# Optimization experiments

Measured on AMD Instinct MI355X. Metric: run time of the kernel, lower is better.

Reference implementation:

```python
import jax, jax.numpy as jnp
import numpy as np

B, T, D, H = 2, 2048, 512, 8
HD = D // H
EPS = 1e-5


def setup_inputs() -> dict:
    key = jax.random.key(0)
    ks = jax.random.split(key, 8)
    s = 1.0 / np.sqrt(D)
    return {
        "x": jax.random.normal(ks[0], (B, T, D), dtype=jnp.float32),
        "Wq": jax.random.uniform(ks[1], (D, D), jnp.float32, -s, s),
        "bq": jnp.zeros((D,), jnp.float32),
        "Wk": jax.random.uniform(ks[2], (D, D), jnp.float32, -s, s),
        "bk": jnp.zeros((D,), jnp.float32),
        "Wv": jax.random.uniform(ks[3], (D, D), jnp.float32, -s, s),
        "bv": jnp.zeros((D,), jnp.float32),
        "gn_w": jnp.ones((D,), jnp.float32),
        "gn_b": jnp.zeros((D,), jnp.float32),
        "gamma": jnp.float32(0.9),
    }


def reference(x, Wq, bq, Wk, bk, Wv, bv, gn_w, gn_b, gamma):
    Bx, Tx, Dx = x.shape
    # projections (torch Linear: x @ W.T + b), split heads -> [B,H,T,hd]
    def proj(W, b):
        return (x @ W.T + b).reshape(Bx, Tx, H, HD).transpose(0, 2, 1, 3)
    Q, K, V = proj(Wq, bq), proj(Wk, bk), proj(Wv, bv)
    # retention scores with causal exponential decay mask
    attn = jnp.einsum("bhqd,bhkd->bhqk", Q, K)  # [B,H,T,T]
    idx = jnp.arange(Tx)
    diff = idx[:, None] - idx[None, :]
    # clamp negative exponents before pow to avoid inf (masked out anyway)
    decay = jnp.where(diff >= 0,
                      jnp.power(gamma, jnp.maximum(diff, 0).astype(jnp.float32)),
                      0.0)
    attn = attn * decay[None, None]
    out = jnp.einsum("bhqk,bhkd->bhqd", attn, V)  # [B,H,T,hd]
    out = out.transpose(0, 2, 1, 3)  # [B,T,H,hd]
    # GroupNorm over channels grouped by head; normalized over (T, hd) per (b, h)
    mean = out.mean(axis=(1, 3), keepdims=True)
    var = out.var(axis=(1, 3), keepdims=True)
    out = (out - mean) / jnp.sqrt(var + EPS)
    out = out.reshape(Bx, Tx, Dx) * gn_w + gn_b
    return out
```

## Files before the change

kernel.cpp:

```cpp
#include <hip/hip_runtime.h>
#include <math.h>

#define B_ 2
#define T_ 2048
#define D_ 512
#define H_ 8
#define HD_ 64
#define NG_ (B_*H_)
#define EPS_ 1e-5f

typedef __attribute__((ext_vector_type(8)))  short  short8;
typedef __attribute__((ext_vector_type(16))) float  floatx16;

__device__ inline floatx16 zero16() {
    floatx16 z;
#pragma unroll
    for (int i = 0; i < 16; i++) z[i] = 0.f;
    return z;
}

__device__ inline unsigned pack2bf(float a, float b) {
    unsigned ua = __float_as_uint(a), ub = __float_as_uint(b);
    ua = (ua + 0x7fffu + ((ua >> 16) & 1u)) >> 16;
    ub = (ub + 0x7fffu + ((ub >> 16) & 1u)) >> 16;
    return ua | (ub << 16);
}
__device__ inline short bf1(float a) {
    unsigned ua = __float_as_uint(a);
    return (short)((ua + 0x7fffu + ((ua >> 16) & 1u)) >> 16);
}

__global__ __launch_bounds__(256) void convert_kernel(
    const float* __restrict__ x,
    const float* __restrict__ Wq, const float* __restrict__ Wk, const float* __restrict__ Wv,
    short* __restrict__ xb, short* __restrict__ Wb)
{
    const int XN = 4096 * 512;
    const int WN = 512 * 512;
    size_t e = ((size_t)blockIdx.x * 256 + threadIdx.x) * 8;
    const float* src; short* dst;
    if (e < XN)               { src = x  + e;               dst = xb + e; }
    else if (e < XN + WN)     { src = Wq + (e - XN);        dst = Wb + (e - XN); }
    else if (e < XN + 2*WN)   { src = Wk + (e - XN - WN);   dst = Wb + (e - XN); }
    else                      { src = Wv + (e - XN - 2*WN); dst = Wb + (e - XN); }
    float4 a = *(const float4*)src;
    float4 b = *(const float4*)(src + 4);
    uint4 o;
    o.x = pack2bf(a.x, a.y); o.y = pack2bf(a.z, a.w);
    o.z = pack2bf(b.x, b.y); o.w = pack2bf(b.z, b.w);
    *(uint4*)dst = o;
}

__global__ __launch_bounds__(256) void proj_mfma(
    const short* __restrict__ xb, const short* __restrict__ Wb,
    const float* __restrict__ bq, const float* __restrict__ bk, const float* __restrict__ bv,
    short* __restrict__ Qo, short* __restrict__ Ko, short* __restrict__ Vto)
{
    __shared__ short Xs[2][64 * 64];
    __shared__ short Ws2[2][128 * 64];

    const int tid = threadIdx.x;
    const int w = tid >> 6, lane = tid & 63;
    const int hi = lane >> 5, ln = lane & 31;
    const int mt0 = blockIdx.x * 64;
    const int nt0 = blockIdx.y * 128;
    const int z = blockIdx.z;
    const bool isV = (z == 2);
    const float* bias = (z == 0) ? bq : (z == 1) ? bk : bv;
    const short* Wz = Wb + (size_t)z * 512 * 512;

    const int srow = tid >> 3;
    const int scol = (tid & 7) * 8;
    const int mh = w & 1, nh = w >> 1;

    floatx16 acc[2] = {zero16(), zero16()};

    auto stage = [&](int b, int k0) {
#pragma unroll
        for (int i = 0; i < 2; i++) {
            const short* gx = xb + (size_t)(mt0 + srow + i * 32) * 512 + k0 + scol;
            short* lx = &Xs[b][(srow + i * 32) * 64 + scol];
            __builtin_amdgcn_global_load_lds(
                (const __attribute__((address_space(1))) unsigned*)gx,
                (__attribute__((address_space(3))) unsigned*)lx, 16, 0, 0);
        }
#pragma unroll
        for (int i = 0; i < 4; i++) {
            const short* gw = Wz + (size_t)(nt0 + srow + i * 32) * 512 + k0 + scol;
            short* lw = &Ws2[b][(srow + i * 32) * 64 + scol];
            __builtin_amdgcn_global_load_lds(
                (const __attribute__((address_space(1))) unsigned*)gw,
                (__attribute__((address_space(3))) unsigned*)lw, 16, 0, 0);
        }
    };

    stage(0, 0);
    int buf = 0;
    for (int k0 = 0; k0 < 512; k0 += 64, buf ^= 1) {
        __syncthreads();
        if (k0 + 64 < 512) stage(buf ^ 1, k0 + 64);
#pragma unroll
        for (int kk = 0; kk < 4; kk++) {
            short8 xf = *(const short8*)(&Xs[buf][(mh * 32 + ln) * 64 + kk * 16 + hi * 8]);
            short8 wf[2];
#pragma unroll
            for (int s = 0; s < 2; s++)
                wf[s] = *(const short8*)(&Ws2[buf][(nh * 64 + s * 32 + ln) * 64 + kk * 16 + hi * 8]);
#pragma unroll
            for (int b = 0; b < 2; b++)
                acc[b] = isV
                    ? __builtin_amdgcn_mfma_f32_32x32x16_bf16(wf[b], xf, acc[b], 0, 0, 0)
                    : __builtin_amdgcn_mfma_f32_32x32x16_bf16(xf, wf[b], acc[b], 0, 0, 0);
        }
    }

    const int head = blockIdx.y * 2 + nh;

    if (!isV) {
        short* dst = (z == 0) ? Qo : Ko;
        float bias_v[2];
#pragma unroll
        for (int b = 0; b < 2; b++) bias_v[b] = bias[nt0 + nh * 64 + b * 32 + ln];
#pragma unroll
        for (int r = 0; r < 16; r++) {
            int m = mt0 + mh * 32 + (r & 3) + 8 * (r >> 2) + 4 * hi;
            int batch = m >> 11, t = m & (T_ - 1);
            size_t rowb = ((size_t)(batch * H_ + head) * T_ + t) * HD_;
#pragma unroll
            for (int b = 0; b < 2; b++)
                dst[rowb + b * 32 + ln] = bf1(acc[b][r] + bias_v[b]);
        }
    } else {
        const int m = mt0 + mh * 32 + ln;
        const int batch = m >> 11, t = m & (T_ - 1);
#pragma unroll
        for (int b = 0; b < 2; b++) {
#pragma unroll
            for (int r = 0; r < 16; r++) {
                int chan = nt0 + nh * 64 + b * 32 + (r & 3) + 8 * (r >> 2) + 4 * hi;
                int d = chan & (HD_ - 1);
                Vto[((size_t)(batch * H_ + head) * HD_ + d) * T_ + t] = bf1(acc[b][r] + bias[chan]);
            }
        }
    }
}

__global__ __launch_bounds__(256, 2) void retention_kernel(
    const short* __restrict__ Q, const short* __restrict__ K, const short* __restrict__ Vt,
    const float* __restrict__ gamma_p,
    float* __restrict__ out,
    float* __restrict__ stats)
{
    __shared__ float red[3][32 * 64];

    const int tid  = threadIdx.x;
    const int ks   = tid >> 6, lane = tid & 63;
    const int hi   = lane >> 5, ln = lane & 31;
    const int g    = blockIdx.x, qtt = blockIdx.y;
    const int q0   = qtt * 32;
    const int qt   = qtt >> 1;

    const float gamma = gamma_p[0];
    const float lg = logf(gamma);
    int kt0 = 0;
    if (lg < -1e-6f) {
        int maxd = (int)(-34.0f / lg) + 64;
        kt0 = qt - (maxd >> 6);
        if (kt0 < 0) kt0 = 0;
    }

    const short* Qbase = Q + ((size_t)g * T_ + q0 + ln) * HD_;
    short8 qf[4];
#pragma unroll
    for (int c = 0; c < 4; c++) qf[c] = *(const short8*)(Qbase + 16 * c + 8 * hi);

    const float Alane = __expf(lg * (float)(ln - 4 * hi));
    const float G32   = __expf(-lg * 32.0f);
    float Ea[4], Eb[4];
#pragma unroll
    for (int j = 0; j < 4; j++) { Ea[j] = __expf(-lg * (float)j); Eb[j] = __expf(-lg * (float)(8 * j)); }
    const int qrel = (qtt & 1) * 32 + ln;

    floatx16 oacc[2] = {zero16(), zero16()};

    int kt = kt0 + ((ks - kt0) & 3);
    short8 kf[2][4];
    if (kt <= qt) {
        const short* Kbase = K + ((size_t)g * T_ + kt * 64) * HD_;
#pragma unroll
        for (int kh = 0; kh < 2; kh++)
#pragma unroll
            for (int c = 0; c < 4; c++)
                kf[kh][c] = *(const short8*)(Kbase + (size_t)(kh * 32 + ln) * HD_ + 16 * c + 8 * hi);
    }

    for (; kt <= qt; kt += 4) {
        const int k0 = kt * 64;

        floatx16 st[2];
#pragma unroll
        for (int kh = 0; kh < 2; kh++) {
            floatx16 acc = zero16();
#pragma unroll
            for (int c = 0; c < 4; c++)
                acc = __builtin_amdgcn_mfma_f32_32x32x16_bf16(kf[kh][c], qf[c], acc, 0, 0, 0);
            st[kh] = acc;
        }

        short8 vf[4][2];
#pragma unroll
        for (int c = 0; c < 4; c++)
#pragma unroll
            for (int dh = 0; dh < 2; dh++)
                vf[c][dh] = *(const short8*)(Vt + ((size_t)g * HD_ + dh * 32 + ln) * T_ + k0 + 16 * c + 8 * hi);

        const int ktn = kt + 4;
        if (ktn <= qt) {
            const short* Kn = K + ((size_t)g * T_ + ktn * 64) * HD_;
#pragma unroll
            for (int kh = 0; kh < 2; kh++)
#pragma unroll
                for (int c = 0; c < 4; c++)
                    kf[kh][c] = *(const short8*)(Kn + (size_t)(kh * 32 + ln) * HD_ + 16 * c + 8 * hi);
        }

        const float Ckt = __expf(lg * (float)(q0 - k0));
        const float base0 = Alane * Ckt;
        const bool diag = (kt == qt);
#pragma unroll
        for (int kh = 0; kh < 2; kh++) {
            float bb = base0 * (kh ? G32 : 1.0f);
#pragma unroll
            for (int r = 0; r < 16; r++) {
                float v = st[kh][r] * (bb * Ea[r & 3] * Eb[r >> 2]);
                if (diag) {
                    int kloc = kh * 32 + (r & 3) + 8 * (r >> 2) + 4 * hi;
                    if (qrel < kloc) v = 0.f;
                }
                st[kh][r] = v;
            }
        }

#pragma unroll
        for (int c = 0; c < 4; c++) {
            const int kh = c >> 1, rb = 8 * (c & 1);
            unsigned p0 = pack2bf(st[kh][rb+0], st[kh][rb+1]);
            unsigned p1 = pack2bf(st[kh][rb+2], st[kh][rb+3]);
            unsigned p2 = pack2bf(st[kh][rb+4], st[kh][rb+5]);
            unsigned p3 = pack2bf(st[kh][rb+6], st[kh][rb+7]);
            unsigned t0s = (unsigned)__shfl_xor((int)(hi ? p0 : p2), 32, 64);
            unsigned t1s = (unsigned)__shfl_xor((int)(hi ? p1 : p3), 32, 64);
            uint4 aw;
            aw.x = hi ? t0s : p0;  aw.y = hi ? t1s : p1;
            aw.z = hi ? p2  : t0s; aw.w = hi ? p3  : t1s;
            short8 afr = *reinterpret_cast<short8*>(&aw);
#pragma unroll
            for (int dh = 0; dh < 2; dh++)
                oacc[dh] = __builtin_amdgcn_mfma_f32_32x32x16_bf16(afr, vf[c][dh], oacc[dh], 0, 0, 0);
        }
    }

    if (ks) {
        float* rp = &red[ks - 1][0];
#pragma unroll
        for (int dh = 0; dh < 2; dh++)
#pragma unroll
            for (int r = 0; r < 16; r++) {
                int qloc = (r & 3) + 8 * (r >> 2) + 4 * hi;
                rp[qloc * 64 + dh * 32 + ln] = oacc[dh][r];
            }
    }
    __syncthreads();
    if (ks == 0) {
        const int b = g >> 3, h = g & 7;
        float sm = 0.f, sq = 0.f;
#pragma unroll
        for (int dh = 0; dh < 2; dh++)
#pragma unroll
            for (int r = 0; r < 16; r++) {
                int qloc = (r & 3) + 8 * (r >> 2) + 4 * hi;
                int col = qloc * 64 + dh * 32 + ln;
                float v = oacc[dh][r] + red[0][col] + red[1][col] + red[2][col];
                int q = q0 + qloc;
                out[((size_t)(b * T_ + q)) * D_ + h * 64 + dh * 32 + ln] = v;
                sm += v; sq += v * v;
            }
        for (int off = 32; off > 0; off >>= 1) {
            sm += __shfl_down(sm, off);
            sq += __shfl_down(sq, off);
        }
        if (lane == 0) {
            atomicAdd(&stats[g], sm);
            atomicAdd(&stats[NG_ + g], sq);
        }
    }
}

__global__ __launch_bounds__(256) void norm_kernel(
    float* __restrict__ out, const float* __restrict__ stats,
    const float* __restrict__ gn_w, const float* __restrict__ gn_b)
{
    int idx4 = blockIdx.x * 256 + threadIdx.x;
    if (idx4 >= (B_ * T_ * D_) / 4) return;
    int base = idx4 * 4;
    int c0 = base & (D_ - 1);
    int b = base >> 20;
    int g = b * H_ + (c0 >> 6);
    const float invN = 1.f / (float)(T_ * HD_);
    float mean = stats[g] * invN;
    float var  = stats[NG_ + g] * invN - mean * mean;
    float inv  = rsqrtf(var + EPS_);
    float4 v = *(float4*)&out[base];
    float4 wv = *(const float4*)&gn_w[c0];
    float4 bv = *(const float4*)&gn_b[c0];
    v.x = (v.x - mean) * inv * wv.x + bv.x;
    v.y = (v.y - mean) * inv * wv.y + bv.y;
    v.z = (v.z - mean) * inv * wv.z + bv.z;
    v.w = (v.w - mean) * inv * wv.w + bv.w;
    *(float4*)&out[base] = v;
}

extern "C" void kernel_launch(void* const* d_in, const int* in_sizes, int n_in,
                              void* d_out, int out_size, void* d_ws, size_t ws_size,
                              hipStream_t stream)
{
    const float* x    = (const float*)d_in[0];
    const float* Wq   = (const float*)d_in[1];
    const float* bq   = (const float*)d_in[2];
    const float* Wk   = (const float*)d_in[3];
    const float* bk   = (const float*)d_in[4];
    const float* Wv   = (const float*)d_in[5];
    const float* bv   = (const float*)d_in[6];
    const float* gn_w = (const float*)d_in[7];
    const float* gn_b = (const float*)d_in[8];
    const float* gam  = (const float*)d_in[9];
    float* out = (float*)d_out;

    const size_t per = (size_t)B_ * H_ * T_ * HD_;
    float* stats = (float*)d_ws;
    short* Qw  = (short*)((char*)d_ws + 256);
    short* Kw  = Qw + per;
    short* Vtw = Kw + per;
    short* xb  = Vtw + per;
    short* Wb  = xb + per;

    hipMemsetAsync(stats, 0, 256, stream);
    convert_kernel<<<1408, 256, 0, stream>>>(x, Wq, Wk, Wv, xb, Wb);
    proj_mfma<<<dim3(64, 4, 3), 256, 0, stream>>>(xb, Wb, bq, bk, bv, Qw, Kw, Vtw);
    retention_kernel<<<dim3(16, 64), 256, 0, stream>>>(Qw, Kw, Vtw, gam, out, stats);
    norm_kernel<<<2048, 256, 0, stream>>>(out, stats, gn_w, gn_b);
}
```

Measured before the change: 128.0 us.

## Fuse all stages into one cooperative persistent kernel with grid syncs

Replaces the memset and four separate launches with a single cooperative kernel. Persistent blocks loop over the convert, projection, retention and norm work items, with grid-wide syncs between stages. The aim is to remove launch gaps and tail effects between kernels. In exchange it limits the grid to a few hundred resident blocks, adds grid-barrier cost, and may lower occupancy because the shared memory and register footprint now cover the largest stage.

```diff
diff --git a/kernel.cpp b/kernel.cpp
--- a/kernel.cpp
+++ b/kernel.cpp
@@ -1,5 +1,8 @@
 #include <hip/hip_runtime.h>
+#include <hip/hip_cooperative_groups.h>
 #include <math.h>
+
+namespace cg = cooperative_groups;
 
 #define B_ 2
 #define T_ 2048
@@ -30,294 +33,301 @@
     return (short)((ua + 0x7fffu + ((ua >> 16) & 1u)) >> 16);
 }
 
-__global__ __launch_bounds__(256) void convert_kernel(
+__global__ __launch_bounds__(256, 2) void mega_kernel(
     const float* __restrict__ x,
-    const float* __restrict__ Wq, const float* __restrict__ Wk, const float* __restrict__ Wv,
-    short* __restrict__ xb, short* __restrict__ Wb)
+    const float* __restrict__ Wq, const float* __restrict__ bq,
+    const float* __restrict__ Wk, const float* __restrict__ bk,
+    const float* __restrict__ Wv, const float* __restrict__ bv,
+    const float* __restrict__ gn_w, const float* __restrict__ gn_b,
+    const float* __restrict__ gamma_p,
+    float* __restrict__ out, float* __restrict__ stats,
+    short* __restrict__ xb, short* __restrict__ Wb,
+    short* __restrict__ Qo, short* __restrict__ Ko, short* __restrict__ Vto,
+    int G)
 {
-    const int XN = 4096 * 512;
-    const int WN = 512 * 512;
-    size_t e = ((size_t)blockIdx.x * 256 + threadIdx.x) * 8;
-    const float* src; short* dst;
-    if (e < XN)               { src = x  + e;               dst = xb + e; }
-    else if (e < XN + WN)     { src = Wq + (e - XN);        dst = Wb + (e - XN); }
-    else if (e < XN + 2*WN)   { src = Wk + (e - XN - WN);   dst = Wb + (e - XN); }
-    else                      { src = Wv + (e - XN - 2*WN); dst = Wb + (e - XN); }
-    float4 a = *(const float4*)src;
-    float4 b = *(const float4*)(src + 4);
-    uint4 o;
-    o.x = pack2bf(a.x, a.y); o.y = pack2bf(a.z, a.w);
-    o.z = pack2bf(b.x, b.y); o.w = pack2bf(b.z, b.w);
-    *(uint4*)dst = o;
-}
-
-__global__ __launch_bounds__(256) void proj_mfma(
-    const short* __restrict__ xb, const short* __restrict__ Wb,
-    const float* __restrict__ bq, const float* __restrict__ bk, const float* __restrict__ bv,
-    short* __restrict__ Qo, short* __restrict__ Ko, short* __restrict__ Vto)
-{
-    __shared__ short Xs[2][64 * 64];
-    __shared__ short Ws2[2][128 * 64];
+    cg::grid_group grid = cg::this_grid();
+    __shared__ __align__(16) char smem[49152];
 
     const int tid = threadIdx.x;
+    const int bid = blockIdx.x;
+    const int gsz = G * 256;
     const int w = tid >> 6, lane = tid & 63;
     const int hi = lane >> 5, ln = lane & 31;
-    const int mt0 = blockIdx.x * 64;
-    const int nt0 = blockIdx.y * 128;
-    const int z = blockIdx.z;
-    const bool isV = (z == 2);
-    const float* bias = (z == 0) ? bq : (z == 1) ? bk : bv;
-    const short* Wz = Wb + (size_t)z * 512 * 512;
-
-    const int srow = tid >> 3;
-    const int scol = (tid & 7) * 8;
-    const int mh = w & 1, nh = w >> 1;
-
-    floatx16 acc[2] = {zero16(), zero16()};
-
-    auto stage = [&](int b, int k0) {
-#pragma unroll
-        for (int i = 0; i < 2; i++) {
-            const short* gx = xb + (size_t)(mt0 + srow + i * 32) * 512 + k0 + scol;
-            short* lx = &Xs[b][(srow + i * 32) * 64 + scol];
-            __builtin_amdgcn_global_load_lds(
-                (const __attribute__((address_space(1))) unsigned*)gx,
-                (__attribute__((address_space(3))) unsigned*)lx, 16, 0, 0);
-        }
-#pragma unroll
-        for (int i = 0; i < 4; i++) {
-            const short* gw = Wz + (size_t)(nt0 + srow + i * 32) * 512 + k0 + scol;
-            short* lw = &Ws2[b][(srow + i * 32) * 64 + scol];
-            __builtin_amdgcn_global_load_lds(
-                (const __attribute__((address_space(1))) unsigned*)gw,
-                (__attribute__((address_space(3))) unsigned*)lw, 16, 0, 0);
-        }
-    };
-
-    stage(0, 0);
-    int buf = 0;
-    for (int k0 = 0; k0 < 512; k0 += 64, buf ^= 1) {
-        __syncthreads();
-        if (k0 + 64 < 512) stage(buf ^ 1, k0 + 64);
-#pragma unroll
-        for (int kk = 0; kk < 4; kk++) {
-            short8 xf = *(const short8*)(&Xs[buf][(mh * 32 + ln) * 64 + kk * 16 + hi * 8]);
-            short8 wf[2];
-#pragma unroll
-            for (int s = 0; s < 2; s++)
-                wf[s] = *(const short8*)(&Ws2[buf][(nh * 64 + s * 32 + ln) * 64 + kk * 16 + hi * 8]);
-#pragma unroll
-            for (int b = 0; b < 2; b++)
-                acc[b] = isV
-                    ? __builtin_amdgcn_mfma_f32_32x32x16_bf16(wf[b], xf, acc[b], 0, 0, 0)
-                    : __builtin_amdgcn_mfma_f32_32x32x16_bf16(xf, wf[b], acc[b], 0, 0, 0);
+
+    if (bid == 0 && tid < 32) stats[tid] = 0.f;
+    {
+        const int XN = 4096 * 512, WN = 512 * 512;
+        const int TOT8 = (XN + 3 * WN) / 8;
+        for (int e8 = bid * 256 + tid; e8 < TOT8; e8 += gsz) {
+            size_t e = (size_t)e8 * 8;
+            const float* src; short* dst;
+            if (e < XN)                 { src = x  + e;                 dst = xb + e; }
+            else if (e < XN + WN)       { src = Wq + (e - XN);          dst = Wb + (e - XN); }
+            else if (e < XN + 2u*WN)    { src = Wk + (e - XN - WN);     dst = Wb + (e - XN); }
+            else                        { src = Wv + (e - XN - 2*WN);   dst = Wb + (e - XN); }
+            float4 a = *(const float4*)src;
+            float4 b = *(const float4*)(src + 4);
+            uint4 o;
+            o.x = pack2bf(a.x, a.y); o.y = pack2bf(a.z, a.w);
+            o.z = pack2bf(b.x, b.y); o.w = pack2bf(b.z, b.w);
+            *(uint4*)dst = o;
         }
     }
-
-    const int head = blockIdx.y * 2 + nh;
-
-    if (!isV) {
-        short* dst = (z == 0) ? Qo : Ko;
-        float bias_v[2];
-#pragma unroll
-        for (int b = 0; b < 2; b++) bias_v[b] = bias[nt0 + nh * 64 + b * 32 + ln];
-#pragma unroll
-        for (int r = 0; r < 16; r++) {
-            int m = mt0 + mh * 32 + (r & 3) + 8 * (r >> 2) + 4 * hi;
-            int batch = m >> 11, t = m & (T_ - 1);
-            size_t rowb = ((size_t)(batch * H_ + head) * T_ + t) * HD_;
-#pragma unroll
-            for (int b = 0; b < 2; b++)
-                dst[rowb + b * 32 + ln] = bf1(acc[b][r] + bias_v[b]);
-        }
-    } else {
-        const int m = mt0 + mh * 32 + ln;
-        const int batch = m >> 11, t = m & (T_ - 1);
-#pragma unroll
-        for (int b = 0; b < 2; b++) {
-#pragma unroll
-            for (int r = 0; r < 16; r++) {
-                int chan = nt0 + nh * 64 + b * 32 + (r & 3) + 8 * (r >> 2) + 4 * hi;
-                int d = chan & (HD_ - 1);
-                Vto[((size_t)(batch * H_ + head) * HD_ + d) * T_ + t] = bf1(acc[b][r] + bias[chan]);
+    grid.sync();
+
+    {
+        short* XsB = (short*)smem;
+        short* WsB = (short*)(smem + 16384);
+        const int srow = tid >> 3, scol = (tid & 7) * 8;
+        const int mh = w & 1, nh = w >> 1;
+
+        for (int job = bid; job < 768; job += G) {
+            const int bx = job & 63, by = (job >> 6) & 3, z = job >> 8;
+            const int mt0 = bx * 64, nt0 = by * 128;
+            const bool isV = (z == 2);
+            const float* bias = (z == 0) ? bq : (z == 1) ? bk : bv;
+            const short* Wz = Wb + (size_t)z * 512 * 512;
+
+            __syncthreads();
+
+            floatx16 acc[2] = {zero16(), zero16()};
+
+            auto stage = [&](int b, int k0) {
+#pragma unroll
+                for (int i = 0; i < 2; i++) {
+                    const short* gx = xb + (size_t)(mt0 + srow + i * 32) * 512 + k0 + scol;
+                    short* lx = XsB + b * 4096 + (srow + i * 32) * 64 + scol;
+                    __builtin_amdgcn_global_load_lds(
+                        (const __attribute__((address_space(1))) unsigned*)gx,
+                        (__attribute__((address_space(3))) unsigned*)lx, 16, 0, 0);
+                }
+#pragma unroll
+                for (int i = 0; i < 4; i++) {
+                    const short* gw = Wz + (size_t)(nt0 + srow + i * 32) * 512 + k0 + scol;
+                    short* lw = WsB + b * 8192 + (srow + i * 32) * 64 + scol;
+                    __builtin_amdgcn_global_load_lds(
+                        (const __attribute__((address_space(1))) unsigned*)gw,
+                        (__attribute__((address_space(3))) unsigned*)lw, 16, 0, 0);
+                }
+            };
+
+            stage(0, 0);
+            int buf = 0;
+            for (int k0 = 0; k0 < 512; k0 += 64, buf ^= 1) {
+                __syncthreads();
+                if (k0 + 64 < 512) stage(buf ^ 1, k0 + 64);
+#pragma unroll
+                for (int kk = 0; kk < 4; kk++) {
+                    short8 xf = *(const short8*)(XsB + buf * 4096 + (mh * 32 + ln) * 64 + kk * 16 + hi * 8);
+                    short8 wf[2];
+#pragma unroll
+                    for (int s = 0; s < 2; s++)
+                        wf[s] = *(const short8*)(WsB + buf * 8192 + (nh * 64 + s * 32 + ln) * 64 + kk * 16 + hi * 8);
+#pragma unroll
+                    for (int b = 0; b < 2; b++)
+                        acc[b] = isV
+                            ? __builtin_amdgcn_mfma_f32_32x32x16_bf16(wf[b], xf, acc[b], 0, 0, 0)
+                            : __builtin_amdgcn_mfma_f32_32x32x16_bf16(xf, wf[b], acc[b], 0, 0, 0);
+                }
+            }
+
+            const int head = by * 2 + nh;
+            if (!isV) {
+                short* dst = (z == 0) ? Qo : Ko;
+                float bias_v[2];
+#pragma unroll
+                for (int b = 0; b < 2; b++) bias_v[b] = bias[nt0 + nh * 64 + b * 32 + ln];
+#pragma unroll
+                for (int r = 0; r < 16; r++) {
+                    int m = mt0 + mh * 32 + (r & 3) + 8 * (r >> 2) + 4 * hi;
+                    int batch = m >> 11, t = m & (T_ - 1);
+                    size_t rowb = ((size_t)(batch * H_ + head) * T_ + t) * HD_;
+#pragma unroll
+                    for (int b = 0; b < 2; b++)
+                        dst[rowb + b * 32 + ln] = bf1(acc[b][r] + bias_v[b]);
+                }
+            } else {
+                const int m = mt0 + mh * 32 + ln;
+                const int batch = m >> 11, t = m & (T_ - 1);
+#pragma unroll
+                for (int b = 0; b < 2; b++) {
+#pragma unroll
+                    for (int r = 0; r < 16; r++) {
+                        int chan = nt0 + nh * 64 + b * 32 + (r & 3) + 8 * (r >> 2) + 4 * hi;
+                        int d = chan & (HD_ - 1);
+                        Vto[((size_t)(batch * H_ + head) * HD_ + d) * T_ + t] = bf1(acc[b][r] + bias[chan]);
+                    }
+                }
             }
         }
     }
-}
-
-__global__ __launch_bounds__(256, 2) void retention_kernel(
-    const short* __restrict__ Q, const short* __restrict__ K, const short* __restrict__ Vt,
-    const float* __restrict__ gamma_p,
-    float* __restrict__ out,
-    float* __restrict__ stats)
-{
-    __shared__ float red[3][32 * 64];
-
-    const int tid  = threadIdx.x;
-    const int ks   = tid >> 6, lane = tid & 63;
-    const int hi   = lane >> 5, ln = lane & 31;
-    const int g    = blockIdx.x, qtt = blockIdx.y;
-    const int q0   = qtt * 32;
-    const int qt   = qtt >> 1;
-
-    const float gamma = gamma_p[0];
-    const float lg = logf(gamma);
-    int kt0 = 0;
-    if (lg < -1e-6f) {
-        int maxd = (int)(-34.0f / lg) + 64;
-        kt0 = qt - (maxd >> 6);
-        if (kt0 < 0) kt0 = 0;
-    }
-
-    const short* Qbase = Q + ((size_t)g * T_ + q0 + ln) * HD_;
-    short8 qf[4];
-#pragma unroll
-    for (int c = 0; c < 4; c++) qf[c] = *(const short8*)(Qbase + 16 * c + 8 * hi);
-
-    const float Alane = __expf(lg * (float)(ln - 4 * hi));
-    const float G32   = __expf(-lg * 32.0f);
-    float Ea[4], Eb[4];
-#pragma unroll
-    for (int j = 0; j < 4; j++) { Ea[j] = __expf(-lg * (float)j); Eb[j] = __expf(-lg * (float)(8 * j)); }
-    const int qrel = (qtt & 1) * 32 + ln;
-
-    floatx16 oacc[2] = {zero16(), zero16()};
-
-    int kt = kt0 + ((ks - kt0) & 3);
-    short8 kf[2][4];
-    if (kt <= qt) {
-        const short* Kbase = K + ((size_t)g * T_ + kt * 64) * HD_;
-#pragma unroll
-        for (int kh = 0; kh < 2; kh++)
-#pragma unroll
-            for (int c = 0; c < 4; c++)
-                kf[kh][c] = *(const short8*)(Kbase + (size_t)(kh * 32 + ln) * HD_ + 16 * c + 8 * hi);
-    }
-
-    for (; kt <= qt; kt += 4) {
-        const int k0 = kt * 64;
-
-        floatx16 st[2];
-#pragma unroll
-        for (int kh = 0; kh < 2; kh++) {
-            floatx16 acc = zero16();
-#pragma unroll
-            for (int c = 0; c < 4; c++)
-                acc = __builtin_amdgcn_mfma_f32_32x32x16_bf16(kf[kh][c], qf[c], acc, 0, 0, 0);
-            st[kh] = acc;
-        }
-
-        short8 vf[4][2];
-#pragma unroll
-        for (int c = 0; c < 4; c++)
-#pragma unroll
-            for (int dh = 0; dh < 2; dh++)
-                vf[c][dh] = *(const short8*)(Vt + ((size_t)g * HD_ + dh * 32 + ln) * T_ + k0 + 16 * c + 8 * hi);
-
-        const int ktn = kt + 4;
-        if (ktn <= qt) {
-            const short* Kn = K + ((size_t)g * T_ + ktn * 64) * HD_;
-#pragma unroll
-            for (int kh = 0; kh < 2; kh++)
+    grid.sync();
+
+    {
+        float* red = (float*)smem;
+        const float gamma = gamma_p[0];
+        const float lg = logf(gamma);
+        const float Alane = __expf(lg * (float)(ln - 4 * hi));
+        const float G32   = __expf(-lg * 32.0f);
+        float Ea[4], Eb[4];
+#pragma unroll
+        for (int j = 0; j < 4; j++) { Ea[j] = __expf(-lg * (float)j); Eb[j] = __expf(-lg * (float)(8 * j)); }
+
+        int ktw = 0;
+        if (lg < -1e-6f) ktw = ((int)(-34.0f / lg) + 64) >> 6;
+
+        for (int job = bid; job < 1024; job += G) {
+            const int g = job & 15, qtt = job >> 4;
+            const int q0 = qtt * 32;
+            const int qt = qtt >> 1;
+            const int ks = w;
+            int kt0 = qt - ktw; if (kt0 < 0) kt0 = 0;
+            const int qrel = (qtt & 1) * 32 + ln;
+
+            __syncthreads();
+
+            const short* Qbase = Qo + ((size_t)g * T_ + q0 + ln) * HD_;
+            short8 qf[4];
+#pragma unroll
+            for (int c = 0; c < 4; c++) qf[c] = *(const short8*)(Qbase + 16 * c + 8 * hi);
+
+            floatx16 oacc[2] = {zero16(), zero16()};
+
+            int kt = kt0 + ((ks - kt0) & 3);
+            short8 kf[2][4];
+            if (kt <= qt) {
+                const short* Kbase = Ko + ((size_t)g * T_ + kt * 64) * HD_;
+#pragma unroll
+                for (int kh = 0; kh < 2; kh++)
+#pragma unroll
+                    for (int c = 0; c < 4; c++)
+                        kf[kh][c] = *(const short8*)(Kbase + (size_t)(kh * 32 + ln) * HD_ + 16 * c + 8 * hi);
+            }
+
+            for (; kt <= qt; kt += 4) {
+                const int k0 = kt * 64;
+
+                floatx16 st[2];
+#pragma unroll
+                for (int kh = 0; kh < 2; kh++) {
+                    floatx16 acc = zero16();
+#pragma unroll
+                    for (int c = 0; c < 4; c++)
+                        acc = __builtin_amdgcn_mfma_f32_32x32x16_bf16(kf[kh][c], qf[c], acc, 0, 0, 0);
+                    st[kh] = acc;
+                }
+
+                short8 vf[4][2];
 #pragma unroll
                 for (int c = 0; c < 4; c++)
-                    kf[kh][c] = *(const short8*)(Kn + (size_t)(kh * 32 + ln) * HD_ + 16 * c + 8 * hi);
-        }
-
-        const float Ckt = __expf(lg * (float)(q0 - k0));
-        const float base0 = Alane * Ckt;
-        const bool diag = (kt == qt);
-#pragma unroll
-        for (int kh = 0; kh < 2; kh++) {
-            float bb = base0 * (kh ? G32 : 1.0f);
-#pragma unroll
-            for (int r = 0; r < 16; r++) {
-                float v = st[kh][r] * (bb * Ea[r & 3] * Eb[r >> 2]);
-                if (diag) {
-                    int kloc = kh * 32 + (r & 3) + 8 * (r >> 2) + 4 * hi;
-                    if (qrel < kloc) v = 0.f;
-                }
-                st[kh][r] = v;
-            }
-        }
-
-#pragma unroll
-        for (int c = 0; c < 4; c++) {
-            const int kh = c >> 1, rb = 8 * (c & 1);
-            unsigned p0 = pack2bf(st[kh][rb+0], st[kh][rb+1]);
-            unsigned p1 = pack2bf(st[kh][rb+2], st[kh][rb+3]);
-            unsigned p2 = pack2bf(st[kh][rb+4], st[kh][rb+5]);
-            unsigned p3 = pack2bf(st[kh][rb+6], st[kh][rb+7]);
-            unsigned t0s = (unsigned)__shfl_xor((int)(hi ? p0 : p2), 32, 64);
-            unsigned t1s = (unsigned)__shfl_xor((int)(hi ? p1 : p3), 32, 64);
-            uint4 aw;
-            aw.x = hi ? t0s : p0;  aw.y = hi ? t1s : p1;
-            aw.z = hi ? p2  : t0s; aw.w = hi ? p3  : t1s;
-            short8 afr = *reinterpret_cast<short8*>(&aw);
-#pragma unroll
-            for (int dh = 0; dh < 2; dh++)
-                oacc[dh] = __builtin_amdgcn_mfma_f32_32x32x16_bf16(afr, vf[c][dh], oacc[dh], 0, 0, 0);
+#pragma unroll
+                    for (int dh = 0; dh < 2; dh++)
+                        vf[c][dh] = *(const short8*)(Vto + ((size_t)g * HD_ + dh * 32 + ln) * T_ + k0 + 16 * c + 8 * hi);
+
+                const int ktn = kt + 4;
+                if (ktn <= qt) {
+                    const short* Kn = Ko + ((size_t)g * T_ + ktn * 64) * HD_;
+#pragma unroll
+                    for (int kh = 0; kh < 2; kh++)
+#pragma unroll
+                        for (int c = 0; c < 4; c++)
+                            kf[kh][c] = *(const short8*)(Kn + (size_t)(kh * 32 + ln) * HD_ + 16 * c + 8 * hi);
+                }
+
+                const float Ckt = __expf(lg * (float)(q0 - k0));
+                const float base0 = Alane * Ckt;
+                const bool diag = (kt == qt);
+#pragma unroll
+                for (int kh = 0; kh < 2; kh++) {
+                    float bb = base0 * (kh ? G32 : 1.0f);
+#pragma unroll
+                    for (int r = 0; r < 16; r++) {
+                        float v = st[kh][r] * (bb * Ea[r & 3] * Eb[r >> 2]);
+                        if (diag) {
+                            int kloc = kh * 32 + (r & 3) + 8 * (r >> 2) + 4 * hi;
+                            if (qrel < kloc) v = 0.f;
+                        }
+                        st[kh][r] = v;
+                    }
+                }
+
+#pragma unroll
+                for (int c = 0; c < 4; c++) {
+                    const int kh = c >> 1, rb = 8 * (c & 1);
+                    unsigned p0 = pack2bf(st[kh][rb+0], st[kh][rb+1]);
+                    unsigned p1 = pack2bf(st[kh][rb+2], st[kh][rb+3]);
+                    unsigned p2 = pack2bf(st[kh][rb+4], st[kh][rb+5]);
+                    unsigned p3 = pack2bf(st[kh][rb+6], st[kh][rb+7]);
+                    unsigned t0s = (unsigned)__shfl_xor((int)(hi ? p0 : p2), 32, 64);
+                    unsigned t1s = (unsigned)__shfl_xor((int)(hi ? p1 : p3), 32, 64);
+                    uint4 aw;
+                    aw.x = hi ? t0s : p0;  aw.y = hi ? t1s : p1;
+                    aw.z = hi ? p2  : t0s; aw.w = hi ? p3  : t1s;
+                    short8 afr = *reinterpret_cast<short8*>(&aw);
+#pragma unroll
+                    for (int dh = 0; dh < 2; dh++)
+                        oacc[dh] = __builtin_amdgcn_mfma_f32_32x32x16_bf16(afr, vf[c][dh], oacc[dh], 0, 0, 0);
+                }
+            }
+
+            if (ks) {
+                float* rp = red + (ks - 1) * 2048;
+#pragma unroll
+                for (int dh = 0; dh < 2; dh++)
+#pragma unroll
+                    for (int r = 0; r < 16; r++) {
+                        int qloc = (r & 3) + 8 * (r >> 2) + 4 * hi;
+                        rp[qloc * 64 + dh * 32 + ln] = oacc[dh][r];
+                    }
+            }
+            __syncthreads();
+            if (ks == 0) {
+                const int b = g >> 3, h = g & 7;
+                float sm = 0.f, sq = 0.f;
+#pragma unroll
+                for (int dh = 0; dh < 2; dh++)
+#pragma unroll
+                    for (int r = 0; r < 16; r++) {
+                        int qloc = (r & 3) + 8 * (r >> 2) + 4 * hi;
+                        int col = qloc * 64 + dh * 32 + ln;
+                        float v = oacc[dh][r] + red[col] + red[2048 + col] + red[4096 + col];
+                        int q = q0 + qloc;
+                        out[((size_t)(b * T_ + q)) * D_ + h * 64 + dh * 32 + ln] = v;
+                        sm += v; sq += v * v;
+                    }
+                for (int off = 32; off > 0; off >>= 1) {
+                    sm += __shfl_down(sm, off);
+                    sq += __shfl_down(sq, off);
+                }
+                if (lane == 0) {
+                    atomicAdd(&stats[g], sm);
+                    atomicAdd(&stats[NG_ + g], sq);
+                }
+            }
         }
     }
-
-    if (ks) {
-        float* rp = &red[ks - 1][0];
-#pragma unroll
-        for (int dh = 0; dh < 2; dh++)
-#pragma unroll
-            for (int r = 0; r < 16; r++) {
-                int qloc = (r & 3) + 8 * (r >> 2) + 4 * hi;
-                rp[qloc * 64 + dh * 32 + ln] = oacc[dh][r];
-            }
-    }
-    __syncthreads();
-    if (ks == 0) {
-        const int b = g >> 3, h = g & 7;
-        float sm = 0.f, sq = 0.f;
-#pragma unroll
-        for (int dh = 0; dh < 2; dh++)
-#pragma unroll
-            for (int r = 0; r < 16; r++) {
-                int qloc = (r & 3) + 8 * (r >> 2) + 4 * hi;
-                int col = qloc * 64 + dh * 32 + ln;
-                float v = oacc[dh][r] + red[0][col] + red[1][col] + red[2][col];
-                int q = q0 + qloc;
-                out[((size_t)(b * T_ + q)) * D_ + h * 64 + dh * 32 + ln] = v;
-                sm += v; sq += v * v;
-            }
-        for (int off = 32; off > 0; off >>= 1) {
-            sm += __shfl_down(sm, off);
-            sq += __shfl_down(sq, off);
-        }
-        if (lane == 0) {
-            atomicAdd(&stats[g], sm);
-            atomicAdd(&stats[NG_ + g], sq);
+    grid.sync();
+
+    {
+        const float invN = 1.f / (float)(T_ * HD_);
+        for (int idx4 = bid * 256 + tid; idx4 < (B_ * T_ * D_) / 4; idx4 += gsz) {
+            int base = idx4 * 4;
+            int c0 = base & (D_ - 1);
+            int b = base >> 20;
+            int g = b * H_ + (c0 >> 6);
+            float mean = stats[g] * invN;
+            float var  = stats[NG_ + g] * invN - mean * mean;
+            float inv  = rsqrtf(var + EPS_);
+            float4 v = *(float4*)&out[base];
+            float4 wv = *(const float4*)&gn_w[c0];
+            float4 bvv = *(const float4*)&gn_b[c0];
+            v.x = (v.x - mean) * inv * wv.x + bvv.x;
+            v.y = (v.y - mean) * inv * wv.y + bvv.y;
+            v.z = (v.z - mean) * inv * wv.z + bvv.z;
+            v.w = (v.w - mean) * inv * wv.w + bvv.w;
+            *(float4*)&out[base] = v;
         }
     }
-}
-
-__global__ __launch_bounds__(256) void norm_kernel(
-    float* __restrict__ out, const float* __restrict__ stats,
-    const float* __restrict__ gn_w, const float* __restrict__ gn_b)
-{
-    int idx4 = blockIdx.x * 256 + threadIdx.x;
-    if (idx4 >= (B_ * T_ * D_) / 4) return;
-    int base = idx4 * 4;
-    int c0 = base & (D_ - 1);
-    int b = base >> 20;
-    int g = b * H_ + (c0 >> 6);
-    const float invN = 1.f / (float)(T_ * HD_);
-    float mean = stats[g] * invN;
-    float var  = stats[NG_ + g] * invN - mean * mean;
-    float inv  = rsqrtf(var + EPS_);
-    float4 v = *(float4*)&out[base];
-    float4 wv = *(const float4*)&gn_w[c0];
-    float4 bv = *(const float4*)&gn_b[c0];
-    v.x = (v.x - mean) * inv * wv.x + bv.x;
-    v.y = (v.y - mean) * inv * wv.y + bv.y;
-    v.z = (v.z - mean) * inv * wv.z + bv.z;
-    v.w = (v.w - mean) * inv * wv.w + bv.w;
-    *(float4*)&out[base] = v;
 }
 
 extern "C" void kernel_launch(void* const* d_in, const int* in_sizes, int n_in,
@@ -344,9 +354,16 @@
     short* xb  = Vtw + per;
     short* Wb  = xb + per;
 
-    hipMemsetAsync(stats, 0, 256, stream);
-    convert_kernel<<<1408, 256, 0, stream>>>(x, Wq, Wk, Wv, xb, Wb);
-    proj_mfma<<<dim3(64, 4, 3), 256, 0, stream>>>(xb, Wb, bq, bk, bv, Qw, Kw, Vtw);
-    retention_kernel<<<dim3(16, 64), 256, 0, stream>>>(Qw, Kw, Vtw, gam, out, stats);
-    norm_kernel<<<2048, 256, 0, stream>>>(out, stats, gn_w, gn_b);
-}
+    int maxB = 0;
+    hipOccupancyMaxActiveBlocksPerMultiprocessor(&maxB, mega_kernel, 256, 0);
+    int G = maxB * 256;
+    if (G > 512) G = 512;
+    if (G < 256) G = 256;
+
+    void* args[] = {(void*)&x, (void*)&Wq, (void*)&bq, (void*)&Wk, (void*)&bk,
+                    (void*)&Wv, (void*)&bv, (void*)&gn_w, (void*)&gn_b, (void*)&gam,
+                    (void*)&out, (void*)&stats, (void*)&xb, (void*)&Wb,
+                    (void*)&Qw, (void*)&Kw, (void*)&Vtw, (void*)&G};
+    hipLaunchCooperativeKernel((const void*)mega_kernel, dim3(G), dim3(256),
+                               args, 0, stream);
+}
```

Measured after the change: 240.9 us. 1.88x slower.
